# Kernel optimization log

Hardware: AMD Instinct MI355X
Metric: run time of the kernel (lower is better)

The kernel has to match this reference:

```python
import jax, jax.numpy as jnp
import numpy as np

C_IN = 128      # pair channel
C_HID = 32      # per-head hidden dim
H = 4           # heads
INF = 1e9
LN_EPS = 1e-5


def setup_inputs() -> dict:
    key = jax.random.key(0)
    ks = jax.random.split(key, 8)
    B, N = 1, 256
    s = 0.02
    return {
        "x": jax.random.normal(ks[0], (B, N, N, C_IN), dtype=jnp.float32),
        "mask": jnp.ones((B, N, N), dtype=jnp.float32),
        "ln_w": jnp.ones((C_IN,), dtype=jnp.float32),
        "ln_b": jnp.zeros((C_IN,), dtype=jnp.float32),
        "w_b": jax.random.normal(ks[1], (H, C_IN), dtype=jnp.float32) * s,      # triangle-bias linear (no bias)
        "w_q": jax.random.normal(ks[2], (H * C_HID, C_IN), dtype=jnp.float32) * s,
        "w_k": jax.random.normal(ks[3], (H * C_HID, C_IN), dtype=jnp.float32) * s,
        "w_v": jax.random.normal(ks[4], (H * C_HID, C_IN), dtype=jnp.float32) * s,
        "w_g": jax.random.normal(ks[5], (H * C_HID, C_IN), dtype=jnp.float32) * s,
        "b_g": jnp.ones((H * C_HID,), dtype=jnp.float32),
        "w_o": jax.random.normal(ks[6], (C_IN, H * C_HID), dtype=jnp.float32) * s,
        "b_o": jnp.zeros((C_IN,), dtype=jnp.float32),
    }


def reference(x, mask, ln_w, ln_b, w_b, w_q, w_k, w_v, w_g, b_g, w_o, b_o):
    # starting=True -> no transpose
    # LayerNorm over channel dim
    mu = jnp.mean(x, axis=-1, keepdims=True)
    var = jnp.var(x, axis=-1, keepdims=True)
    xn = (x - mu) * jax.lax.rsqrt(var + LN_EPS) * ln_w + ln_b            # [B,I,J,C]

    # mask bias: [B, I, 1, 1, J]
    mask_bias = (INF * (mask - 1.0))[..., :, None, None, :]

    # triangle bias: linear -> [B,I,J,H] -> permute -> [B,H,I,J] -> [B,1,H,I,J]
    tri_bias = jnp.einsum("bijc,hc->bhij", xn, w_b)[:, None]

    # QKV projections, per-head: weights reshaped to [H, D, C]
    Wq = w_q.reshape(H, C_HID, C_IN)
    Wk = w_k.reshape(H, C_HID, C_IN)
    Wv = w_v.reshape(H, C_HID, C_IN)
    scale = 1.0 / np.sqrt(C_HID)
    q = jnp.einsum("bijc,hdc->bihjd", xn, Wq) * scale                    # [B,I,H,J,D]
    k = jnp.einsum("bijc,hdc->bihjd", xn, Wk)
    v = jnp.einsum("bijc,hdc->bihjd", xn, Wv)

    # attention over the J (column) axis of each row i
    a = jnp.einsum("bihqd,bihkd->bihqk", q, k) + mask_bias + tri_bias    # [B,I,H,J,J]
    a = jax.nn.softmax(a, axis=-1)
    o = jnp.einsum("bihqk,bihkd->biqhd", a, v)                           # [B,I,J,H,D]

    # sigmoid gating
    g = jax.nn.sigmoid(jnp.einsum("bijc,ec->bije", xn, w_g) + b_g)       # [B,I,J,H*D]
    o = o.reshape(*o.shape[:-2], H * C_HID) * g

    # output projection
    return jnp.einsum("bije,ce->bijc", o, w_o) + b_o                     # [B,I,J,C_in]
```

## Files before the change

kernel.cpp:

```cpp
#include <hip/hip_runtime.h>

#define N 256
#define C 128
#define H 4
#define D 32
#define NP (N*N)
#define LN_EPS 1e-5f
#define LOG2E 1.4426950408889634f

__device__ __forceinline__ void barrier_lgkm() {
    __asm__ volatile("s_waitcnt lgkmcnt(0)" ::: "memory");
    __builtin_amdgcn_sched_barrier(0);
    __builtin_amdgcn_s_barrier();
    __builtin_amdgcn_sched_barrier(0);
}

using f32x4 = __attribute__((ext_vector_type(4))) float;
using bf8   = __attribute__((ext_vector_type(8))) short;
using u16x4 = __attribute__((ext_vector_type(4))) unsigned short;

__device__ __forceinline__ float bf2f(ushort u) {
    union { uint u; float f; } v; v.u = ((uint)u) << 16; return v.f;
}
__device__ __forceinline__ ushort f2bf(float f) {
    union { float f; uint u; } v; v.f = f;
    uint u = v.u;
    u += 0x7fffu + ((u >> 16) & 1u);
    return (ushort)(u >> 16);
}
__device__ __forceinline__ ushort f2bf_trunc(float f) {
    union { float f; uint u; } v; v.f = f;
    return (ushort)(v.u >> 16);
}

__global__ __launch_bounds__(256) void prep_weights(
    const float* __restrict__ wq, const float* __restrict__ wk,
    const float* __restrict__ wv, const float* __restrict__ wg,
    const float* __restrict__ wb, const float* __restrict__ wo,
    ushort* __restrict__ Wcat, ushort* __restrict__ WbPad, ushort* __restrict__ Wo)
{
    int t = blockIdx.x * 256 + threadIdx.x;
    const float scale = 0.17677669529663689f * LOG2E;
    float v;
    if (t < 16384)       v = wq[t] * scale;
    else if (t < 32768)  v = wk[t - 16384];
    else if (t < 49152)  v = wv[t - 32768];
    else                 v = wg[t - 49152];
    Wcat[t] = f2bf(v);
    if (t < 16384) Wo[t] = f2bf(wo[t]);
    if (t < 2048)  WbPad[t] = (t < 512) ? f2bf(wb[t]) : (ushort)0;
}

__global__ __launch_bounds__(512, 4) void ln_proj(
    const float* __restrict__ x, const float* __restrict__ lnw,
    const float* __restrict__ lnb, const ushort* __restrict__ Wcat,
    const ushort* __restrict__ WbPad, const float* __restrict__ bg,
    ushort* __restrict__ qb, ushort* __restrict__ kb,
    ushort* __restrict__ vbT, ushort* __restrict__ gate,
    ushort* __restrict__ tri_p)
{
    __shared__ ushort At[64 * 128];
    int mt = blockIdx.x;
    int t  = threadIdx.x;
    int wave = t >> 6, lane = t & 63;
    int lane32 = lane & 31, rsel = lane >> 5;

    {
        const float4 w4 = ((const float4*)lnw)[lane32];
        const float4 b4 = ((const float4*)lnb)[lane32];
        const float* xb = x + (size_t)mt * 64 * C;
        float4 xv[4];
        #pragma unroll
        for (int pp = 0; pp < 4; pp++) {
            int r = pp * 16 + wave * 2 + rsel;
            xv[pp] = ((const float4*)(xb + r * C))[lane32];
        }
        #pragma unroll
        for (int pp = 0; pp < 4; pp++) {
            int r = pp * 16 + wave * 2 + rsel;
            float4 v = xv[pp];
            float s  = v.x + v.y + v.z + v.w;
            float ss = v.x*v.x + v.y*v.y + v.z*v.z + v.w*v.w;
            #pragma unroll
            for (int m = 1; m < 32; m <<= 1) {
                s  += __shfl_xor(s, m, 64);
                ss += __shfl_xor(ss, m, 64);
            }
            float mean = s * (1.f / 128.f);
            float var  = ss * (1.f / 128.f) - mean * mean;
            float rstd = rsqrtf(var + LN_EPS);
            u16x4 o;
            o[0] = f2bf((v.x - mean) * rstd * w4.x + b4.x);
            o[1] = f2bf((v.y - mean) * rstd * w4.y + b4.y);
            o[2] = f2bf((v.z - mean) * rstd * w4.z + b4.z);
            o[3] = f2bf((v.w - mean) * rstd * w4.w + b4.w);
            int c8 = lane32 >> 1;
            int chunk = r * 16 + (c8 ^ (r & 7));
            *(u16x4*)&At[chunk * 8 + (lane32 & 1) * 4] = o;
        }
    }
    barrier_lgkm();

    int lrow = lane & 15, quad = lane >> 4;
    int wr = wave >> 2, wc = wave & 3;

    bf8 afr[4][2];
    #pragma unroll
    for (int ks = 0; ks < 4; ks++) {
        int c8 = ks * 4 + quad;
        #pragma unroll
        for (int mi = 0; mi < 2; mi++) {
            int row = wr * 32 + mi * 16 + lrow;
            afr[ks][mi] = *(const bf8*)&At[(row * 16 + (c8 ^ (row & 7))) * 8];
        }
    }

    if (wc == 0) {
        f32x4 at0 = (f32x4){0.f,0.f,0.f,0.f}, at1 = (f32x4){0.f,0.f,0.f,0.f};
        #pragma unroll
        for (int ks = 0; ks < 4; ks++) {
            bf8 bt = *(const bf8*)(WbPad + lrow * C + (ks * 4 + quad) * 8);
            at0 = __builtin_amdgcn_mfma_f32_16x16x32_bf16(afr[ks][0], bt, at0, 0, 0, 0);
            at1 = __builtin_amdgcn_mfma_f32_16x16x32_bf16(afr[ks][1], bt, at1, 0, 0, 0);
        }
        if (lrow < 4) {
            int q = mt >> 2;
            int qc = q >> 4, quadq = (q >> 2) & 3, rr = q & 3;
            #pragma unroll
            for (int mi = 0; mi < 2; mi++) {
                #pragma unroll
                for (int r = 0; r < 4; r++) {
                    int k = (mt & 3) * 64 + wr * 32 + mi * 16 + quad * 4 + r;
                    int n = k >> 4, lk = k & 15;
                    int lanet = quadq * 16 + lk;
                    int v2 = n * 4 + rr, j = v2 >> 3, m2 = v2 & 7;
                    float val = (mi == 0) ? at0[r] : at1[r];
                    tri_p[lrow * 65536 + ((qc * 8 + j) * 64 + lanet) * 8 + m2] =
                        f2bf(val * LOG2E);
                }
            }
        }
    }

    #pragma unroll 1
    for (int nt = 0; nt < 4; nt++) {
        const ushort* Wt = Wcat + (size_t)nt * 128 * C;
        f32x4 acc[2][2];
        #pragma unroll
        for (int mi = 0; mi < 2; mi++)
            #pragma unroll
            for (int ni = 0; ni < 2; ni++) acc[mi][ni] = (f32x4){0.f, 0.f, 0.f, 0.f};

        #pragma unroll
        for (int ks = 0; ks < 4; ks++) {
            int c8 = ks * 4 + quad;
            bf8 b0 = *(const bf8*)(Wt + (size_t)(wc * 32 + lrow)      * C + c8 * 8);
            bf8 b1 = *(const bf8*)(Wt + (size_t)(wc * 32 + 16 + lrow) * C + c8 * 8);
            acc[0][0] = __builtin_amdgcn_mfma_f32_16x16x32_bf16(afr[ks][0], b0, acc[0][0], 0, 0, 0);
            acc[0][1] = __builtin_amdgcn_mfma_f32_16x16x32_bf16(afr[ks][0], b1, acc[0][1], 0, 0, 0);
            acc[1][0] = __builtin_amdgcn_mfma_f32_16x16x32_bf16(afr[ks][1], b0, acc[1][0], 0, 0, 0);
            acc[1][1] = __builtin_amdgcn_mfma_f32_16x16x32_bf16(afr[ks][1], b1, acc[1][1], 0, 0, 0);
        }

        barrier_lgkm();
        if (nt == 2) {
            #pragma unroll
            for (int mi = 0; mi < 2; mi++) {
                #pragma unroll
                for (int ni = 0; ni < 2; ni++) {
                    int col = wc * 32 + ni * 16 + lrow;
                    #pragma unroll
                    for (int r = 0; r < 4; r++) {
                        int keyl = wr * 32 + mi * 16 + quad * 4 + r;
                        At[col * 64 + (keyl ^ ((col & 7) << 3))] = f2bf(acc[mi][ni][r]);
                    }
                }
            }
            barrier_lgkm();
            int i_row = mt >> 2, kq = mt & 3;
            #pragma unroll
            for (int itr = 0; itr < 2; itr++) {
                int oidx = itr * 512 + t;
                int col = oidx >> 3, kc = oidx & 7;
                bf8 val = *(const bf8*)&At[col * 64 + ((kc * 8) ^ ((col & 7) << 3))];
                *(bf8*)&vbT[(size_t)(i_row * 128 + col) * N + kq * 64 + kc * 8] = val;
            }
        } else {
            ushort* dst = (nt == 0) ? qb : (nt == 1) ? kb : gate;
            float g0 = 0.f, g1 = 0.f;
            if (nt == 3) { g0 = bg[wc * 32 + lrow]; g1 = bg[wc * 32 + 16 + lrow]; }
            #pragma unroll
            for (int mi = 0; mi < 2; mi++) {
                #pragma unroll
                for (int ni = 0; ni < 2; ni++) {
                    int col = wc * 32 + ni * 16 + lrow;
                    #pragma unroll
                    for (int r = 0; r < 4; r++) {
                        int row = wr * 32 + mi * 16 + quad * 4 + r;
                        float vv = acc[mi][ni][r];
                        if (nt == 3)
                            vv = 1.f / (1.f + __expf(-(vv + ((ni == 0) ? g0 : g1))));
                        At[(row * 16 + ((col >> 3) ^ (row & 7))) * 8 + (col & 7)] = f2bf(vv);
                    }
                }
            }
            barrier_lgkm();
            #pragma unroll
            for (int itr = 0; itr < 2; itr++) {
                int oidx = itr * 512 + t;
                int row = oidx >> 4, c8 = oidx & 15;
                bf8 val = *(const bf8*)&At[(row * 16 + (c8 ^ (row & 7))) * 8];
                *(bf8*)&dst[(size_t)(mt * 64 + row) * C + c8 * 8] = val;
            }
        }
    }
}

__global__ __launch_bounds__(512, 4) void attn_kernel(
    const ushort* __restrict__ qb, const ushort* __restrict__ kb,
    const ushort* __restrict__ vbT, const ushort* __restrict__ tri_p,
    const float* __restrict__ mask, ushort* __restrict__ ob)
{
    __shared__ ushort Kf[8192];
    __shared__ ushort Vf[8192];
    __shared__ ushort Pf[8][2048];

    int i  = blockIdx.x;
    int h  = blockIdx.y;
    int t  = threadIdx.x;
    int wave = t >> 6, lane = t & 63;
    int lrow = lane & 15, quad = lane >> 4;

    bf8 aqr[2];
    #pragma unroll
    for (int cc = 0; cc < 2; cc++)
        aqr[cc] = *(const bf8*)(qb + (size_t)(i * N + (wave * 2 + cc) * 16 + lrow) * C
                                + h * D + quad * 8);

    {
        const ushort* kt = kb + (size_t)(i * N) * C + h * D;
        #pragma unroll
        for (int it = 0; it < 2; it++) {
            int idx = it * 512 + t;
            int key = idx >> 2, d0 = (idx & 3) * 8;
            bf8 kv = *(const bf8*)(kt + (size_t)key * C + d0);
            int c = (idx >> 6) * 64 + (idx & 3) * 16 + ((idx >> 2) & 15);
            *(bf8*)&Kf[c * 8] = kv;
        }
    }
    {
        const ushort* vt = vbT + (size_t)((i * H + h) * D) * N;
        #pragma unroll
        for (int it = 0; it < 2; it++) {
            int idx = it * 512 + t;
            bf8 vv = *(const bf8*)(vt + idx * 8);
            int c = (idx >> 9) * 512 + ((idx >> 2) & 7) * 64 + (idx & 3) * 16 + ((idx >> 5) & 15);
            c ^= (c >> 6) & 7;
            *(bf8*)&Vf[c * 8] = vv;
        }
    }
    float mb[16];
    #pragma unroll
    for (int n = 0; n < 16; n++)
        mb[n] = (1e9f * LOG2E) * (mask[i * N + n * 16 + lrow] - 1.0f);
    barrier_lgkm();

    ushort* Pw = &Pf[wave][0];
    const ushort* trih = tri_p + (size_t)h * 65536;
    int pq = quad * 32 + (lrow & 7);
    int l3 = (lrow >> 3) & 1;

    #pragma unroll 1
    for (int cc = 0; cc < 2; cc++) {
        int qc = wave * 2 + cc;
        bf8 aq = cc ? aqr[1] : aqr[0];
        float sum[4] = {0.f, 0.f, 0.f, 0.f};
        f32x4 o[2];
        o[0] = (f32x4){0.f, 0.f, 0.f, 0.f};
        o[1] = (f32x4){0.f, 0.f, 0.f, 0.f};

        #pragma unroll
        for (int half = 0; half < 2; half++) {
            f32x4 s8[8];
            __builtin_amdgcn_s_setprio(1);
            #pragma unroll
            for (int n8 = 0; n8 < 8; n8++) {
                bf8 kf = *(const bf8*)&Kf[((half * 8 + n8) * 64 + lane) * 8];
                s8[n8] = __builtin_amdgcn_mfma_f32_16x16x32_bf16(
                    aq, kf, (f32x4){0.f, 0.f, 0.f, 0.f}, 0, 0, 0);
            }
            __builtin_amdgcn_s_setprio(0);
            const ushort* tp = trih + ((size_t)(qc * 8 + half * 4) * 64 + lane) * 8;
            bf8 tf[4];
            #pragma unroll
            for (int jj = 0; jj < 4; jj++)
                tf[jj] = *(const bf8*)(tp + jj * 512);

            #pragma unroll
            for (int n8 = 0; n8 < 8; n8++) {
                int pa = (n8 >> 1) * 512 + (((n8 << 1) + l3) & 3) * 128 + pq;
                #pragma unroll
                for (int r = 0; r < 4; r++) {
                    float tb = bf2f(((const ushort*)&tf[n8 >> 1])[((n8 & 1) << 2) + r]);
                    float e  = exp2f(s8[n8][r] + tb + mb[half * 8 + n8]);
                    sum[r]  += e;
                    Pw[pa + r * 8] = f2bf_trunc(e);
                }
            }
            __asm__ volatile("s_waitcnt lgkmcnt(0)" ::: "memory");
            __builtin_amdgcn_sched_barrier(0);

            __builtin_amdgcn_s_setprio(1);
            #pragma unroll
            for (int ks = 0; ks < 4; ks++) {
                bf8 ap = *(const bf8*)&Pw[(ks * 64 + lane) * 8];
                int ksg = half * 4 + ks;
                #pragma unroll
                for (int nv = 0; nv < 2; nv++) {
                    int c = nv * 512 + ksg * 64 + (lane ^ (ksg & 7));
                    bf8 bv = *(const bf8*)&Vf[c * 8];
                    o[nv] = __builtin_amdgcn_mfma_f32_16x16x32_bf16(ap, bv, o[nv], 0, 0, 0);
                }
            }
            __builtin_amdgcn_s_setprio(0);
        }
        #pragma unroll
        for (int r = 0; r < 4; r++) {
            float s = sum[r];
            s += __shfl_xor(s, 1, 64);
            s += __shfl_xor(s, 2, 64);
            s += __shfl_xor(s, 4, 64);
            s += __shfl_xor(s, 8, 64);
            sum[r] = 1.f / s;
        }
        #pragma unroll
        for (int nv = 0; nv < 2; nv++) {
            int d = nv * 16 + lrow;
            #pragma unroll
            for (int r = 0; r < 4; r++) {
                int qg = qc * 16 + quad * 4 + r;
                ob[(size_t)(i * N + qg) * C + h * D + d] = f2bf(o[nv][r] * sum[r]);
            }
        }
    }
}

__global__ __launch_bounds__(512, 4) void out_gemm(
    const ushort* __restrict__ ob, const ushort* __restrict__ gate,
    const ushort* __restrict__ Wo, const float* __restrict__ bo,
    float* __restrict__ out)
{
    __shared__ ushort At[128 * 128];
    __shared__ ushort Bt[128 * 128];
    int mt = blockIdx.x;
    int t  = threadIdx.x;

    const uint4* Og = (const uint4*)(ob   + (size_t)mt * 128 * C);
    const uint4* Gg = (const uint4*)(gate + (size_t)mt * 128 * C);
    const uint4* Bg = (const uint4*)Wo;
    #pragma unroll
    for (int ii = 0; ii < 4; ii++) {
        int idx = t + ii * 512;
        int row = idx >> 4, c8 = idx & 15;
        int sc = row * 16 + (c8 ^ (row & 7));
        uint4 o4 = Og[idx], g4 = Gg[idx], r4;
        const ushort* os = (const ushort*)&o4;
        const ushort* gs = (const ushort*)&g4;
        ushort* rs = (ushort*)&r4;
        #pragma unroll
        for (int j = 0; j < 8; j++) rs[j] = f2bf(bf2f(os[j]) * bf2f(gs[j]));
        ((uint4*)At)[sc] = r4;
        ((uint4*)Bt)[sc] = Bg[idx];
    }
    barrier_lgkm();

    int wave = t >> 6, lane = t & 63;
    int lrow = lane & 15, quad = lane >> 4;
    int wr = wave >> 1, wc = wave & 1;

    f32x4 acc[2][4];
    #pragma unroll
    for (int mi = 0; mi < 2; mi++)
        #pragma unroll
        for (int ni = 0; ni < 4; ni++) acc[mi][ni] = (f32x4){0.f, 0.f, 0.f, 0.f};

    #pragma unroll
    for (int ks = 0; ks < 4; ks++) {
        int c8 = ks * 4 + quad;
        bf8 a[2], b[4];
        #pragma unroll
        for (int mi = 0; mi < 2; mi++) {
            int row = wr * 32 + mi * 16 + lrow;
            a[mi] = *(const bf8*)&At[(row * 16 + (c8 ^ (row & 7))) * 8];
        }
        #pragma unroll
        for (int ni = 0; ni < 4; ni++) {
            int row = wc * 64 + ni * 16 + lrow;
            b[ni] = *(const bf8*)&Bt[(row * 16 + (c8 ^ (row & 7))) * 8];
        }
        #pragma unroll
        for (int mi = 0; mi < 2; mi++)
            #pragma unroll
            for (int ni = 0; ni < 4; ni++)
                acc[mi][ni] = __builtin_amdgcn_mfma_f32_16x16x32_bf16(a[mi], b[ni], acc[mi][ni], 0, 0, 0);
    }

    #pragma unroll
    for (int mi = 0; mi < 2; mi++) {
        #pragma unroll
        for (int ni = 0; ni < 4; ni++) {
            int col = wc * 64 + ni * 16 + lrow;
            float bias = bo[col];
            #pragma unroll
            for (int r = 0; r < 4; r++) {
                int row = mt * 128 + wr * 32 + mi * 16 + quad * 4 + r;
                out[(size_t)row * C + col] = acc[mi][ni][r] + bias;
            }
        }
    }
}

extern "C" void kernel_launch(void* const* d_in, const int* in_sizes, int n_in,
                              void* d_out, int out_size, void* d_ws, size_t ws_size,
                              hipStream_t stream)
{
    const float* x    = (const float*)d_in[0];
    const float* mask = (const float*)d_in[1];
    const float* lnw  = (const float*)d_in[2];
    const float* lnb  = (const float*)d_in[3];
    const float* wb   = (const float*)d_in[4];
    const float* wq   = (const float*)d_in[5];
    const float* wk   = (const float*)d_in[6];
    const float* wv   = (const float*)d_in[7];
    const float* wg   = (const float*)d_in[8];
    const float* bg   = (const float*)d_in[9];
    const float* wo   = (const float*)d_in[10];
    const float* bo   = (const float*)d_in[11];
    float* out = (float*)d_out;

    uintptr_t w = (uintptr_t)d_ws;
    ushort* qb    = (ushort*)w; w += (size_t)NP * C * 2;
    ushort* kb    = (ushort*)w; w += (size_t)NP * C * 2;
    ushort* vbT   = (ushort*)w; w += (size_t)NP * C * 2;
    ushort* gate  = (ushort*)w; w += (size_t)NP * C * 2;
    ushort* ob    = (ushort*)w; w += (size_t)NP * C * 2;
    ushort* tri_p = (ushort*)w; w += (size_t)H * NP * 2;
    ushort* Wcat  = (ushort*)w; w += 512 * 128 * 2;
    ushort* WbPad = (ushort*)w; w += 16 * 128 * 2;
    ushort* Wo    = (ushort*)w; w += 128 * 128 * 2;

    prep_weights<<<256, 256, 0, stream>>>(wq, wk, wv, wg, wb, wo, Wcat, WbPad, Wo);
    ln_proj<<<NP / 64, 512, 0, stream>>>(x, lnw, lnb, Wcat, WbPad, bg,
                                         qb, kb, vbT, gate, tri_p);
    attn_kernel<<<dim3(N, H), 512, 0, stream>>>(qb, kb, vbT, tri_p, mask, ob);
    out_gemm<<<NP / 128, 512, 0, stream>>>(ob, gate, Wo, bo, out);
}
```

Measured before the change: 184.7 us.

## Fuse gating and output projection into attention kernel, looping heads per block

After: 184.4 us. About the same (-0.2%).

```diff
diff --git a/kernel.cpp b/kernel.cpp
--- a/kernel.cpp
+++ b/kernel.cpp
@@ -216,95 +216,92 @@
     }
 }
 
-__global__ __launch_bounds__(512, 4) void attn_kernel(
+__global__ __launch_bounds__(512, 4) void attn_out(
     const ushort* __restrict__ qb, const ushort* __restrict__ kb,
     const ushort* __restrict__ vbT, const ushort* __restrict__ tri_p,
-    const float* __restrict__ mask, ushort* __restrict__ ob)
+    const float* __restrict__ mask, const ushort* __restrict__ gate,
+    const ushort* __restrict__ Wo, const float* __restrict__ bo,
+    float* __restrict__ out)
 {
     __shared__ ushort Kf[8192];
     __shared__ ushort Vf[8192];
     __shared__ ushort Pf[8][2048];
 
     int i  = blockIdx.x;
-    int h  = blockIdx.y;
+    int qh = blockIdx.y;
     int t  = threadIdx.x;
     int wave = t >> 6, lane = t & 63;
     int lrow = lane & 15, quad = lane >> 4;
-
-    bf8 aqr[2];
-    #pragma unroll
-    for (int cc = 0; cc < 2; cc++)
-        aqr[cc] = *(const bf8*)(qb + (size_t)(i * N + (wave * 2 + cc) * 16 + lrow) * C
-                                + h * D + quad * 8);
-
-    {
-        const ushort* kt = kb + (size_t)(i * N) * C + h * D;
-        #pragma unroll
-        for (int it = 0; it < 2; it++) {
-            int idx = it * 512 + t;
-            int key = idx >> 2, d0 = (idx & 3) * 8;
-            bf8 kv = *(const bf8*)(kt + (size_t)key * C + d0);
-            int c = (idx >> 6) * 64 + (idx & 3) * 16 + ((idx >> 2) & 15);
-            *(bf8*)&Kf[c * 8] = kv;
-        }
-    }
-    {
-        const ushort* vt = vbT + (size_t)((i * H + h) * D) * N;
-        #pragma unroll
-        for (int it = 0; it < 2; it++) {
-            int idx = it * 512 + t;
-            bf8 vv = *(const bf8*)(vt + idx * 8);
-            int c = (idx >> 9) * 512 + ((idx >> 2) & 7) * 64 + (idx & 3) * 16 + ((idx >> 5) & 15);
-            c ^= (c >> 6) & 7;
-            *(bf8*)&Vf[c * 8] = vv;
-        }
-    }
+    int qc = qh * 8 + wave;
+
     float mb[16];
     #pragma unroll
     for (int n = 0; n < 16; n++)
         mb[n] = (1e9f * LOG2E) * (mask[i * N + n * 16 + lrow] - 1.0f);
-    barrier_lgkm();
+
+    f32x4 oacc[8];
+    #pragma unroll
+    for (int ct = 0; ct < 8; ct++) oacc[ct] = (f32x4){0.f, 0.f, 0.f, 0.f};
 
     ushort* Pw = &Pf[wave][0];
-    const ushort* trih = tri_p + (size_t)h * 65536;
-    int pq = quad * 32 + (lrow & 7);
-    int l3 = (lrow >> 3) & 1;
+    const int pq = quad * 32 + (lrow & 7);
+    const int l3 = (lrow >> 3) & 1;
 
     #pragma unroll 1
-    for (int cc = 0; cc < 2; cc++) {
-        int qc = wave * 2 + cc;
-        bf8 aq = cc ? aqr[1] : aqr[0];
+    for (int h = 0; h < 4; h++) {
+        bf8 aq = *(const bf8*)(qb + (size_t)(i * N + qc * 16 + lrow) * C
+                               + h * D + quad * 8);
+        barrier_lgkm();
+        {
+            const ushort* kt = kb + (size_t)(i * N) * C + h * D;
+            #pragma unroll
+            for (int it = 0; it < 2; it++) {
+                int idx = it * 512 + t;
+                int key = idx >> 2, d0 = (idx & 3) * 8;
+                bf8 kv = *(const bf8*)(kt + (size_t)key * C + d0);
+                int c = (idx >> 6) * 64 + (idx & 3) * 16 + ((idx >> 2) & 15);
+                *(bf8*)&Kf[c * 8] = kv;
+            }
+        }
+        {
+            const ushort* vt = vbT + (size_t)((i * H + h) * D) * N;
+            #pragma unroll
+            for (int it = 0; it < 2; it++) {
+                int idx = it * 512 + t;
+                bf8 vv = *(const bf8*)(vt + idx * 8);
+                int c = (idx >> 9) * 512 + ((idx >> 2) & 7) * 64 + (idx & 3) * 16 + ((idx >> 5) & 15);
+                c ^= (c >> 6) & 7;
+                *(bf8*)&Vf[c * 8] = vv;
+            }
+        }
+        barrier_lgkm();
+
         float sum[4] = {0.f, 0.f, 0.f, 0.f};
         f32x4 o[2];
         o[0] = (f32x4){0.f, 0.f, 0.f, 0.f};
         o[1] = (f32x4){0.f, 0.f, 0.f, 0.f};
+        const ushort* trih = tri_p + (size_t)h * 65536;
 
         #pragma unroll
         for (int half = 0; half < 2; half++) {
-            f32x4 s8[8];
-            __builtin_amdgcn_s_setprio(1);
-            #pragma unroll
-            for (int n8 = 0; n8 < 8; n8++) {
-                bf8 kf = *(const bf8*)&Kf[((half * 8 + n8) * 64 + lane) * 8];
-                s8[n8] = __builtin_amdgcn_mfma_f32_16x16x32_bf16(
-                    aq, kf, (f32x4){0.f, 0.f, 0.f, 0.f}, 0, 0, 0);
-            }
-            __builtin_amdgcn_s_setprio(0);
             const ushort* tp = trih + ((size_t)(qc * 8 + half * 4) * 64 + lane) * 8;
-            bf8 tf[4];
-            #pragma unroll
-            for (int jj = 0; jj < 4; jj++)
-                tf[jj] = *(const bf8*)(tp + jj * 512);
-
-            #pragma unroll
-            for (int n8 = 0; n8 < 8; n8++) {
-                int pa = (n8 >> 1) * 512 + (((n8 << 1) + l3) & 3) * 128 + pq;
+            #pragma unroll
+            for (int p = 0; p < 4; p++) {
+                bf8 tf = *(const bf8*)(tp + p * 512);
                 #pragma unroll
-                for (int r = 0; r < 4; r++) {
-                    float tb = bf2f(((const ushort*)&tf[n8 >> 1])[((n8 & 1) << 2) + r]);
-                    float e  = exp2f(s8[n8][r] + tb + mb[half * 8 + n8]);
-                    sum[r]  += e;
-                    Pw[pa + r * 8] = f2bf_trunc(e);
+                for (int j = 0; j < 2; j++) {
+                    int n8 = p * 2 + j;
+                    bf8 kf = *(const bf8*)&Kf[((half * 8 + n8) * 64 + lane) * 8];
+                    f32x4 s = __builtin_amdgcn_mfma_f32_16x16x32_bf16(
+                        aq, kf, (f32x4){0.f, 0.f, 0.f, 0.f}, 0, 0, 0);
+                    int pa = (n8 >> 1) * 512 + (((n8 << 1) + l3) & 3) * 128 + pq;
+                    #pragma unroll
+                    for (int r = 0; r < 4; r++) {
+                        float tb = bf2f(((const ushort*)&tf)[j * 4 + r]);
+                        float e  = exp2f(s[r] + tb + mb[half * 8 + n8]);
+                        sum[r]  += e;
+                        Pw[pa + r * 8] = f2bf_trunc(e);
+                    }
                 }
             }
             __asm__ volatile("s_waitcnt lgkmcnt(0)" ::: "memory");
@@ -324,6 +321,7 @@
             }
             __builtin_amdgcn_s_setprio(0);
         }
+
         #pragma unroll
         for (int r = 0; r < 4; r++) {
             float s = sum[r];
@@ -333,89 +331,36 @@
             s += __shfl_xor(s, 8, 64);
             sum[r] = 1.f / s;
         }
+        const ushort* gt = gate + (size_t)(i * N + qc * 16) * C + h * D;
         #pragma unroll
         for (int nv = 0; nv < 2; nv++) {
-            int d = nv * 16 + lrow;
             #pragma unroll
             for (int r = 0; r < 4; r++) {
-                int qg = qc * 16 + quad * 4 + r;
-                ob[(size_t)(i * N + qg) * C + h * D + d] = f2bf(o[nv][r] * sum[r]);
-            }
-        }
-    }
-}
-
-__global__ __launch_bounds__(512, 4) void out_gemm(
-    const ushort* __restrict__ ob, const ushort* __restrict__ gate,
-    const ushort* __restrict__ Wo, const float* __restrict__ bo,
-    float* __restrict__ out)
-{
-    __shared__ ushort At[128 * 128];
-    __shared__ ushort Bt[128 * 128];
-    int mt = blockIdx.x;
-    int t  = threadIdx.x;
-
-    const uint4* Og = (const uint4*)(ob   + (size_t)mt * 128 * C);
-    const uint4* Gg = (const uint4*)(gate + (size_t)mt * 128 * C);
-    const uint4* Bg = (const uint4*)Wo;
+                float g = bf2f(gt[(quad * 4 + r) * C + nv * 16 + lrow]);
+                float val = o[nv][r] * sum[r] * g;
+                Pw[(nv * 2 + l3) * 128 + pq + r * 8] = f2bf(val);
+            }
+        }
+        __asm__ volatile("s_waitcnt lgkmcnt(0)" ::: "memory");
+        __builtin_amdgcn_sched_barrier(0);
+
+        bf8 ap = *(const bf8*)&Pw[lane * 8];
+        __builtin_amdgcn_s_setprio(1);
+        #pragma unroll
+        for (int ct = 0; ct < 8; ct++) {
+            bf8 wv = *(const bf8*)(Wo + (size_t)(ct * 16 + lrow) * 128 + h * D + quad * 8);
+            oacc[ct] = __builtin_amdgcn_mfma_f32_16x16x32_bf16(ap, wv, oacc[ct], 0, 0, 0);
+        }
+        __builtin_amdgcn_s_setprio(0);
+    }
+
     #pragma unroll
-    for (int ii = 0; ii < 4; ii++) {
-        int idx = t + ii * 512;
-        int row = idx >> 4, c8 = idx & 15;
-        int sc = row * 16 + (c8 ^ (row & 7));
-        uint4 o4 = Og[idx], g4 = Gg[idx], r4;
-        const ushort* os = (const ushort*)&o4;
-        const ushort* gs = (const ushort*)&g4;
-        ushort* rs = (ushort*)&r4;
-        #pragma unroll
-        for (int j = 0; j < 8; j++) rs[j] = f2bf(bf2f(os[j]) * bf2f(gs[j]));
-        ((uint4*)At)[sc] = r4;
-        ((uint4*)Bt)[sc] = Bg[idx];
-    }
-    barrier_lgkm();
-
-    int wave = t >> 6, lane = t & 63;
-    int lrow = lane & 15, quad = lane >> 4;
-    int wr = wave >> 1, wc = wave & 1;
-
-    f32x4 acc[2][4];
-    #pragma unroll
-    for (int mi = 0; mi < 2; mi++)
-        #pragma unroll
-        for (int ni = 0; ni < 4; ni++) acc[mi][ni] = (f32x4){0.f, 0.f, 0.f, 0.f};
-
-    #pragma unroll
-    for (int ks = 0; ks < 4; ks++) {
-        int c8 = ks * 4 + quad;
-        bf8 a[2], b[4];
-        #pragma unroll
-        for (int mi = 0; mi < 2; mi++) {
-            int row = wr * 32 + mi * 16 + lrow;
-            a[mi] = *(const bf8*)&At[(row * 16 + (c8 ^ (row & 7))) * 8];
-        }
-        #pragma unroll
-        for (int ni = 0; ni < 4; ni++) {
-            int row = wc * 64 + ni * 16 + lrow;
-            b[ni] = *(const bf8*)&Bt[(row * 16 + (c8 ^ (row & 7))) * 8];
-        }
-        #pragma unroll
-        for (int mi = 0; mi < 2; mi++)
-            #pragma unroll
-            for (int ni = 0; ni < 4; ni++)
-                acc[mi][ni] = __builtin_amdgcn_mfma_f32_16x16x32_bf16(a[mi], b[ni], acc[mi][ni], 0, 0, 0);
-    }
-
-    #pragma unroll
-    for (int mi = 0; mi < 2; mi++) {
-        #pragma unroll
-        for (int ni = 0; ni < 4; ni++) {
-            int col = wc * 64 + ni * 16 + lrow;
-            float bias = bo[col];
-            #pragma unroll
-            for (int r = 0; r < 4; r++) {
-                int row = mt * 128 + wr * 32 + mi * 16 + quad * 4 + r;
-                out[(size_t)row * C + col] = acc[mi][ni][r] + bias;
-            }
+    for (int ct = 0; ct < 8; ct++) {
+        float bias = bo[ct * 16 + lrow];
+        #pragma unroll
+        for (int r = 0; r < 4; r++) {
+            int qg = qc * 16 + quad * 4 + r;
+            out[(size_t)(i * N + qg) * C + ct * 16 + lrow] = oacc[ct][r] + bias;
         }
     }
 }
@@ -443,7 +388,6 @@
     ushort* kb    = (ushort*)w; w += (size_t)NP * C * 2;
     ushort* vbT   = (ushort*)w; w += (size_t)NP * C * 2;
     ushort* gate  = (ushort*)w; w += (size_t)NP * C * 2;
-    ushort* ob    = (ushort*)w; w += (size_t)NP * C * 2;
     ushort* tri_p = (ushort*)w; w += (size_t)H * NP * 2;
     ushort* Wcat  = (ushort*)w; w += 512 * 128 * 2;
     ushort* WbPad = (ushort*)w; w += 16 * 128 * 2;
@@ -452,6 +396,6 @@
     prep_weights<<<256, 256, 0, stream>>>(wq, wk, wv, wg, wb, wo, Wcat, WbPad, Wo);
     ln_proj<<<NP / 64, 512, 0, stream>>>(x, lnw, lnb, Wcat, WbPad, bg,
                                          qb, kb, vbT, gate, tri_p);
-    attn_kernel<<<dim3(N, H), 512, 0, stream>>>(qb, kb, vbT, tri_p, mask, ob);
-    out_gemm<<<NP / 128, 512, 0, stream>>>(ob, gate, Wo, bo, out);
-}
+    attn_out<<<dim3(N, 2), 512, 0, stream>>>(qb, kb, vbT, tri_p, mask, gate,
+                                             Wo, bo, out);
+}
```
